# Performance work log

Measured on AMD Instinct MI355X. Metric: run time of the kernel, lower is better.

The kernel has to match this reference:

```python
import jax, jax.numpy as jnp
import numpy as np

B, C, D, H, W = 4, 128, 32, 32, 32
EMB, K = 64, 512


def setup_inputs() -> dict:
    key = jax.random.key(0)
    k1, k2, k3 = jax.random.split(key, 3)
    x = jax.random.normal(k1, (B, C, D, H, W), dtype=jnp.float32)
    conv_w = jax.random.normal(k2, (EMB, C), dtype=jnp.float32) * 0.05  # 1x1x1 Conv3d kernel
    conv_b = jnp.zeros((EMB,), dtype=jnp.float32)
    embed = jax.random.normal(k3, (EMB, K), dtype=jnp.float32)  # codebook, (dim, n_embed)
    return {"x": x, "conv_w": conv_w, "conv_b": conv_b, "embed": embed}


def reference(x, conv_w, conv_b, embed):
    # 1x1x1 Conv3d == per-voxel linear projection; permute to channels-last
    z = jnp.einsum('bcdhw,oc->bdhwo', x, conv_w) + conv_b  # (B,D,H,W,EMB)
    emb_dim = embed.shape[0]
    flat = z.reshape(-1, emb_dim)  # (N, EMB)
    # squared euclidean distance to each codebook entry: ||f||^2 - 2 f.e + ||e||^2
    dist = (jnp.sum(flat * flat, axis=1, keepdims=True)
            - 2.0 * (flat @ embed)
            + jnp.sum(embed * embed, axis=0, keepdims=True))  # (N, K)
    embed_ind = jnp.argmin(dist, axis=1)  # (N,)
    embed_ind = embed_ind.reshape(z.shape[:-1])  # (B,D,H,W)
    quantize = jnp.take(embed.T, embed_ind, axis=0)  # (B,D,H,W,EMB) gather
    diff = jnp.mean((jax.lax.stop_gradient(quantize) - z) ** 2)
    quantize = z + jax.lax.stop_gradient(quantize - z)  # straight-through
    return quantize.transpose(0, 4, 1, 2, 3), diff, embed_ind
```

## Files before the change

### kernel.cpp

```cpp
#include <hip/hip_runtime.h>
#include <hip/hip_bf16.h>

#define CIN   128
#define EMBD  64
#define KC    512
#define SPAT  32768
#define NVOX  131072
#define QSZ   (NVOX * EMBD)
#define DIFF_OFF QSZ
#define IDX_OFF  (QSZ + 1)

__global__ __launch_bounds__(64) void vq_prep(const float* __restrict__ embed,
                                              float* __restrict__ embedT,
                                              float* __restrict__ norms) {
  int k = blockIdx.x;
  int o = threadIdx.x;
  float e = embed[o * KC + k];
  embedT[k * EMBD + o] = e;
  float s = e * e;
  #pragma unroll
  for (int off = 32; off > 0; off >>= 1) s += __shfl_down(s, off);
  if (o == 0) norms[k] = s;
}

__global__ __launch_bounds__(256, 2) void vq_main(
    const float* __restrict__ x, const float* __restrict__ conv_w,
    const float* __restrict__ conv_b, const float* __restrict__ embedT,
    const float* __restrict__ norms, float* __restrict__ out,
    float* __restrict__ partials) {
  __shared__ float wlds[CIN * 68];
  for (int f = threadIdx.x; f < CIN * EMBD; f += 256) {
    int o = f >> 7;
    int c = f & (CIN - 1);
    wlds[c * 68 + o] = conv_w[f];
  }
  __syncthreads();

  const int n = blockIdx.x * 256 + threadIdx.x;
  const int b = n >> 15;
  const int v = n & (SPAT - 1);
  const float* xp = x + ((size_t)b * CIN) * SPAT + v;

  float z[EMBD];
  #pragma unroll
  for (int o = 0; o < EMBD; ++o) z[o] = conv_b[o];

  for (int c = 0; c < CIN; ++c) {
    float xv = xp[(size_t)c * SPAT];
    const float* wr = &wlds[c * 68];
    #pragma unroll
    for (int o = 0; o < EMBD; ++o) z[o] = fmaf(xv, wr[o], z[o]);
  }

  float best = 3.4e38f;
  int bi = 0;
  for (int k = 0; k < KC; ++k) {
    const float* ek = embedT + k * EMBD;
    float d0 = 0.f, d1 = 0.f, d2 = 0.f, d3 = 0.f;
    #pragma unroll
    for (int o = 0; o < EMBD; o += 4) {
      float4 e4 = *(const float4*)(ek + o);
      d0 = fmaf(z[o + 0], e4.x, d0);
      d1 = fmaf(z[o + 1], e4.y, d1);
      d2 = fmaf(z[o + 2], e4.z, d2);
      d3 = fmaf(z[o + 3], e4.w, d3);
    }
    float dot = (d0 + d1) + (d2 + d3);
    float s = fmaf(-2.f, dot, norms[k]);
    if (s < best) { best = s; bi = k; }
  }

  const float* eb = embedT + bi * EMBD;
  float* qout = out + ((size_t)b * EMBD) * SPAT + v;
  float diff = 0.f;
  #pragma unroll
  for (int o = 0; o < EMBD; ++o) {
    float e = eb[o];
    float r = e - z[o];
    diff = fmaf(r, r, diff);
    qout[(size_t)o * SPAT] = e;
  }
  out[IDX_OFF + n] = (float)bi;

  #pragma unroll
  for (int off = 32; off > 0; off >>= 1) diff += __shfl_down(diff, off);
  __syncthreads();
  if ((threadIdx.x & 63) == 0) wlds[threadIdx.x >> 6] = diff;
  __syncthreads();
  if (threadIdx.x == 0)
    partials[blockIdx.x] = wlds[0] + wlds[1] + wlds[2] + wlds[3];
}

__global__ __launch_bounds__(512) void vq_final(const float* __restrict__ partials,
                                                float* __restrict__ out) {
  __shared__ float tmp[8];
  float s = partials[threadIdx.x];
  #pragma unroll
  for (int off = 32; off > 0; off >>= 1) s += __shfl_down(s, off);
  if ((threadIdx.x & 63) == 0) tmp[threadIdx.x >> 6] = s;
  __syncthreads();
  if (threadIdx.x == 0) {
    float t = 0.f;
    #pragma unroll
    for (int i = 0; i < 8; ++i) t += tmp[i];
    out[DIFF_OFF] = t * (1.0f / (float)QSZ);
  }
}

extern "C" void kernel_launch(void* const* d_in, const int* in_sizes, int n_in,
                              void* d_out, int out_size, void* d_ws, size_t ws_size,
                              hipStream_t stream) {
  const float* x      = (const float*)d_in[0];
  const float* conv_w = (const float*)d_in[1];
  const float* conv_b = (const float*)d_in[2];
  const float* embed  = (const float*)d_in[3];
  float* out = (float*)d_out;
  float* ws  = (float*)d_ws;

  float* embedT   = ws;
  float* norms    = ws + 32768;
  float* partials = ws + 33280;

  vq_prep<<<KC, EMBD, 0, stream>>>(embed, embedT, norms);
  vq_main<<<NVOX / 256, 256, 0, stream>>>(x, conv_w, conv_b, embedT, norms,
                                          out, partials);
  vq_final<<<1, 512, 0, stream>>>(partials, out);
}
```

Before: 352.8 us.

## Split embedding dimension across half-waves to cut registers and raise occupancy

Each voxel is now handled by two lanes that each own 32 of the 64 embedding channels, with the partial distance dot product combined through a cross-half shuffle. This halves the per-thread z array, allowing launch bounds of 4 waves per SIMD, and doubles the grid. In exchange each codebook entry needs an extra shuffle per lane, and the x loads are duplicated across the two halves. The LDS weight padding is removed and the final reduction now reads 1024 partials.

```diff
diff --git a/kernel.cpp b/kernel.cpp
--- a/kernel.cpp
+++ b/kernel.cpp
@@ -23,78 +23,88 @@
   if (o == 0) norms[k] = s;
 }
 
-__global__ __launch_bounds__(256, 2) void vq_main(
+__global__ __launch_bounds__(256, 4) void vq_main(
     const float* __restrict__ x, const float* __restrict__ conv_w,
     const float* __restrict__ conv_b, const float* __restrict__ embedT,
     const float* __restrict__ norms, float* __restrict__ out,
     float* __restrict__ partials) {
-  __shared__ float wlds[CIN * 68];
+  __shared__ float wlds[CIN * EMBD];
   for (int f = threadIdx.x; f < CIN * EMBD; f += 256) {
     int o = f >> 7;
     int c = f & (CIN - 1);
-    wlds[c * 68 + o] = conv_w[f];
+    wlds[c * EMBD + o] = conv_w[f];
   }
   __syncthreads();
 
-  const int n = blockIdx.x * 256 + threadIdx.x;
-  const int b = n >> 15;
-  const int v = n & (SPAT - 1);
+  const int tid   = threadIdx.x;
+  const int wv    = tid >> 6;
+  const int lane  = tid & 63;
+  const int h     = lane >> 5;
+  const int vloc  = lane & 31;
+  const int n     = blockIdx.x * 128 + wv * 32 + vloc;
+  const int b     = n >> 15;
+  const int v     = n & (SPAT - 1);
+  const int obase = h * 32;
+
   const float* xp = x + ((size_t)b * CIN) * SPAT + v;
 
-  float z[EMBD];
+  float z[32];
   #pragma unroll
-  for (int o = 0; o < EMBD; ++o) z[o] = conv_b[o];
+  for (int i = 0; i < 32; ++i) z[i] = conv_b[obase + i];
 
+  #pragma unroll 4
   for (int c = 0; c < CIN; ++c) {
     float xv = xp[(size_t)c * SPAT];
-    const float* wr = &wlds[c * 68];
+    const float* wr = &wlds[c * EMBD + obase];
     #pragma unroll
-    for (int o = 0; o < EMBD; ++o) z[o] = fmaf(xv, wr[o], z[o]);
+    for (int i = 0; i < 32; ++i) z[i] = fmaf(xv, wr[i], z[i]);
   }
 
   float best = 3.4e38f;
   int bi = 0;
+  #pragma unroll 2
   for (int k = 0; k < KC; ++k) {
-    const float* ek = embedT + k * EMBD;
+    const float* ek = embedT + k * EMBD + obase;
     float d0 = 0.f, d1 = 0.f, d2 = 0.f, d3 = 0.f;
     #pragma unroll
-    for (int o = 0; o < EMBD; o += 4) {
-      float4 e4 = *(const float4*)(ek + o);
-      d0 = fmaf(z[o + 0], e4.x, d0);
-      d1 = fmaf(z[o + 1], e4.y, d1);
-      d2 = fmaf(z[o + 2], e4.z, d2);
-      d3 = fmaf(z[o + 3], e4.w, d3);
+    for (int q = 0; q < 8; ++q) {
+      float4 e4 = *(const float4*)(ek + q * 4);
+      d0 = fmaf(z[q * 4 + 0], e4.x, d0);
+      d1 = fmaf(z[q * 4 + 1], e4.y, d1);
+      d2 = fmaf(z[q * 4 + 2], e4.z, d2);
+      d3 = fmaf(z[q * 4 + 3], e4.w, d3);
     }
     float dot = (d0 + d1) + (d2 + d3);
+    dot += __shfl_xor(dot, 32);
     float s = fmaf(-2.f, dot, norms[k]);
     if (s < best) { best = s; bi = k; }
   }
 
-  const float* eb = embedT + bi * EMBD;
-  float* qout = out + ((size_t)b * EMBD) * SPAT + v;
+  const float* eb = embedT + bi * EMBD + obase;
+  float* qout = out + ((size_t)b * EMBD + obase) * SPAT + v;
   float diff = 0.f;
   #pragma unroll
-  for (int o = 0; o < EMBD; ++o) {
-    float e = eb[o];
-    float r = e - z[o];
+  for (int i = 0; i < 32; ++i) {
+    float e = eb[i];
+    float r = e - z[i];
     diff = fmaf(r, r, diff);
-    qout[(size_t)o * SPAT] = e;
+    qout[(size_t)i * SPAT] = e;
   }
-  out[IDX_OFF + n] = (float)bi;
+  if (h == 0) out[IDX_OFF + n] = (float)bi;
 
   #pragma unroll
   for (int off = 32; off > 0; off >>= 1) diff += __shfl_down(diff, off);
   __syncthreads();
-  if ((threadIdx.x & 63) == 0) wlds[threadIdx.x >> 6] = diff;
+  if (lane == 0) wlds[wv] = diff;
   __syncthreads();
-  if (threadIdx.x == 0)
+  if (tid == 0)
     partials[blockIdx.x] = wlds[0] + wlds[1] + wlds[2] + wlds[3];
 }
 
 __global__ __launch_bounds__(512) void vq_final(const float* __restrict__ partials,
                                                 float* __restrict__ out) {
   __shared__ float tmp[8];
-  float s = partials[threadIdx.x];
+  float s = partials[threadIdx.x] + partials[threadIdx.x + 512];
   #pragma unroll
   for (int off = 32; off > 0; off >>= 1) s += __shfl_down(s, off);
   if ((threadIdx.x & 63) == 0) tmp[threadIdx.x >> 6] = s;
@@ -122,7 +132,7 @@
   float* partials = ws + 33280;
 
   vq_prep<<<KC, EMBD, 0, stream>>>(embed, embedT, norms);
-  vq_main<<<NVOX / 256, 256, 0, stream>>>(x, conv_w, conv_b, embedT, norms,
+  vq_main<<<NVOX / 128, 256, 0, stream>>>(x, conv_w, conv_b, embedT, norms,
                                           out, partials);
   vq_final<<<1, 512, 0, stream>>>(partials, out);
 }
```

Measured after the change: 640.3 us. +81.5%, slower.

## Compute codebook distances with split-bf16 MFMA and per-block voxel tiling

Applied to the files above, without the earlier changes.

Replaces the scalar per-thread distance loop over all 512 codes with bf16 MFMA matrix products. Both z and the codebook are split into hi/mid/lo bf16 parts, and six cross-product passes approximate fp32 precision. Each block now handles 64 voxels, with the 4 waves each owning 128 codes and 16 output channels. Argmin is reduced via shuffles and LDS, and diff is computed from best distance plus ||z||^2. This removes the heavy VALU dot-product cost, but risks argmin ties or precision mismatches and adds extra prep kernels.

```diff
diff --git a/kernel.cpp b/kernel.cpp
--- a/kernel.cpp
+++ b/kernel.cpp
@@ -9,92 +9,227 @@
 #define QSZ   (NVOX * EMBD)
 #define DIFF_OFF QSZ
 #define IDX_OFF  (QSZ + 1)
-
-__global__ __launch_bounds__(64) void vq_prep(const float* __restrict__ embed,
-                                              float* __restrict__ embedT,
-                                              float* __restrict__ norms) {
+#define NBLK  (NVOX / 64)
+
+typedef __attribute__((ext_vector_type(8))) short bf16x8;
+typedef __attribute__((ext_vector_type(4))) float f32x4;
+
+__device__ __forceinline__ short bf_hi(float f) {
+  __hip_bfloat16 h = __float2bfloat16(f);
+  return *(short*)&h;
+}
+__device__ __forceinline__ float bf_f(short s) {
+  __hip_bfloat16 h = *(__hip_bfloat16*)&s;
+  return __bfloat162float(h);
+}
+
+__global__ __launch_bounds__(64) void vq_prep_e(const float* __restrict__ embed,
+                                                float* __restrict__ embedT,
+                                                float* __restrict__ norms,
+                                                short* __restrict__ e_h,
+                                                short* __restrict__ e_m,
+                                                short* __restrict__ e_l) {
   int k = blockIdx.x;
   int o = threadIdx.x;
   float e = embed[o * KC + k];
   embedT[k * EMBD + o] = e;
+  short h = bf_hi(e);
+  float r1 = e - bf_f(h);
+  short m = bf_hi(r1);
+  short l = bf_hi(r1 - bf_f(m));
+  e_h[k * EMBD + o] = h;
+  e_m[k * EMBD + o] = m;
+  e_l[k * EMBD + o] = l;
   float s = e * e;
   #pragma unroll
   for (int off = 32; off > 0; off >>= 1) s += __shfl_down(s, off);
   if (o == 0) norms[k] = s;
 }
 
+__global__ __launch_bounds__(256) void vq_prep_w(const float* __restrict__ conv_w,
+                                                 float* __restrict__ wT) {
+  int f = blockIdx.x * 256 + threadIdx.x;
+  int c = f >> 6;
+  int o = f & 63;
+  wT[f] = conv_w[o * CIN + c];
+}
+
 __global__ __launch_bounds__(256, 2) void vq_main(
-    const float* __restrict__ x, const float* __restrict__ conv_w,
+    const float* __restrict__ x, const float* __restrict__ wT,
     const float* __restrict__ conv_b, const float* __restrict__ embedT,
-    const float* __restrict__ norms, float* __restrict__ out,
-    float* __restrict__ partials) {
-  __shared__ float wlds[CIN * 68];
-  for (int f = threadIdx.x; f < CIN * EMBD; f += 256) {
-    int o = f >> 7;
-    int c = f & (CIN - 1);
-    wlds[c * 68 + o] = conv_w[f];
-  }
-  __syncthreads();
-
-  const int n = blockIdx.x * 256 + threadIdx.x;
-  const int b = n >> 15;
-  const int v = n & (SPAT - 1);
-  const float* xp = x + ((size_t)b * CIN) * SPAT + v;
-
-  float z[EMBD];
-  #pragma unroll
-  for (int o = 0; o < EMBD; ++o) z[o] = conv_b[o];
-
+    const short* __restrict__ e_h, const short* __restrict__ e_m,
+    const short* __restrict__ e_l, const float* __restrict__ norms,
+    float* __restrict__ out, float* __restrict__ partials) {
+  __shared__ short zh[64 * 64], zm[64 * 64], zl[64 * 64];
+  __shared__ float norml[KC];
+  __shared__ float zsq4[64][4];
+  __shared__ float wbest[4][64];
+  __shared__ int   widx[4][64];
+  __shared__ int   fidx[64];
+
+  const int t    = threadIdx.x;
+  const int q    = t >> 6;
+  const int v    = t & 63;
+  const int n0   = blockIdx.x * 64;
+  const int b    = n0 >> 15;
+  const int vsp  = n0 & (SPAT - 1);
+
+  norml[t]       = norms[t];
+  norml[t + 256] = norms[t + 256];
+
+  const float* xp = x + ((size_t)b * CIN) * SPAT + vsp + v;
+  float z[16];
+  #pragma unroll
+  for (int j = 0; j < 16; ++j) z[j] = conv_b[q * 16 + j];
+
+  #pragma unroll 4
   for (int c = 0; c < CIN; ++c) {
     float xv = xp[(size_t)c * SPAT];
-    const float* wr = &wlds[c * 68];
-    #pragma unroll
-    for (int o = 0; o < EMBD; ++o) z[o] = fmaf(xv, wr[o], z[o]);
-  }
-
-  float best = 3.4e38f;
-  int bi = 0;
-  for (int k = 0; k < KC; ++k) {
-    const float* ek = embedT + k * EMBD;
-    float d0 = 0.f, d1 = 0.f, d2 = 0.f, d3 = 0.f;
-    #pragma unroll
-    for (int o = 0; o < EMBD; o += 4) {
-      float4 e4 = *(const float4*)(ek + o);
-      d0 = fmaf(z[o + 0], e4.x, d0);
-      d1 = fmaf(z[o + 1], e4.y, d1);
-      d2 = fmaf(z[o + 2], e4.z, d2);
-      d3 = fmaf(z[o + 3], e4.w, d3);
-    }
-    float dot = (d0 + d1) + (d2 + d3);
-    float s = fmaf(-2.f, dot, norms[k]);
-    if (s < best) { best = s; bi = k; }
-  }
-
-  const float* eb = embedT + bi * EMBD;
-  float* qout = out + ((size_t)b * EMBD) * SPAT + v;
-  float diff = 0.f;
-  #pragma unroll
-  for (int o = 0; o < EMBD; ++o) {
-    float e = eb[o];
-    float r = e - z[o];
-    diff = fmaf(r, r, diff);
-    qout[(size_t)o * SPAT] = e;
-  }
-  out[IDX_OFF + n] = (float)bi;
-
-  #pragma unroll
-  for (int off = 32; off > 0; off >>= 1) diff += __shfl_down(diff, off);
-  __syncthreads();
-  if ((threadIdx.x & 63) == 0) wlds[threadIdx.x >> 6] = diff;
-  __syncthreads();
-  if (threadIdx.x == 0)
-    partials[blockIdx.x] = wlds[0] + wlds[1] + wlds[2] + wlds[3];
+    const float* wr = wT + c * EMBD + q * 16;
+    #pragma unroll
+    for (int j = 0; j < 16; ++j) z[j] = fmaf(xv, wr[j], z[j]);
+  }
+
+  float sq = 0.f;
+  #pragma unroll
+  for (int j = 0; j < 16; ++j) sq = fmaf(z[j], z[j], sq);
+  zsq4[v][q] = sq;
+
+  short h16[16], m16[16], l16[16];
+  #pragma unroll
+  for (int j = 0; j < 16; ++j) {
+    short h = bf_hi(z[j]);
+    float r1 = z[j] - bf_f(h);
+    short m = bf_hi(r1);
+    h16[j] = h; m16[j] = m; l16[j] = bf_hi(r1 - bf_f(m));
+  }
+  #pragma unroll
+  for (int jj = 0; jj < 2; ++jj) {
+    int s = (2 * q + jj) ^ (v & 7);
+    int byte = v * 128 + s * 16;
+    bf16x8 hv, mv, lv;
+    #pragma unroll
+    for (int j = 0; j < 8; ++j) { hv[j] = h16[jj*8+j]; mv[j] = m16[jj*8+j]; lv[j] = l16[jj*8+j]; }
+    *(bf16x8*)((char*)zh + byte) = hv;
+    *(bf16x8*)((char*)zm + byte) = mv;
+    *(bf16x8*)((char*)zl + byte) = lv;
+  }
+  __syncthreads();
+
+  const int lane = t & 63;
+  const int l15  = lane & 15;
+  const int g    = lane >> 4;
+
+  f32x4 acc[4][8];
+  #pragma unroll
+  for (int m = 0; m < 4; ++m)
+    #pragma unroll
+    for (int n = 0; n < 8; ++n) { f32x4 z4 = {0.f,0.f,0.f,0.f}; acc[m][n] = z4; }
+
+  const int boff = (q * 128 + l15) * 128 + g * 16;
+
+  auto dist_pass = [&](const short* zlds, const short* __restrict__ eg) {
+    #pragma unroll
+    for (int ks8 = 0; ks8 <= 4; ks8 += 4) {
+      bf16x8 a[4];
+      #pragma unroll
+      for (int m = 0; m < 4; ++m) {
+        int vox = m * 16 + l15;
+        a[m] = *(const bf16x8*)((const char*)zlds + vox * 128 +
+                                (((ks8 + g) ^ (vox & 7)) << 4));
+      }
+      #pragma unroll
+      for (int n = 0; n < 8; ++n) {
+        bf16x8 bb = *(const bf16x8*)((const char*)eg + boff + n * 2048 + ks8 * 16);
+        #pragma unroll
+        for (int m = 0; m < 4; ++m)
+          acc[m][n] = __builtin_amdgcn_mfma_f32_16x16x32_bf16(a[m], bb, acc[m][n], 0, 0, 0);
+      }
+    }
+  };
+  dist_pass(zh, e_h);
+  dist_pass(zh, e_m);
+  dist_pass(zm, e_h);
+  dist_pass(zh, e_l);
+  dist_pass(zl, e_h);
+  dist_pass(zm, e_m);
+
+  float nv[8];
+  #pragma unroll
+  for (int n = 0; n < 8; ++n) nv[n] = norml[q * 128 + n * 16 + l15];
+
+  float best[16]; int bidx[16];
+  #pragma unroll
+  for (int i = 0; i < 16; ++i) { best[i] = 3.4e38f; bidx[i] = 0; }
+  #pragma unroll
+  for (int n = 0; n < 8; ++n)
+    #pragma unroll
+    for (int m = 0; m < 4; ++m)
+      #pragma unroll
+      for (int r = 0; r < 4; ++r) {
+        float s = fmaf(-2.f, acc[m][n][r], nv[n]);
+        int code = q * 128 + n * 16 + l15;
+        int i = m * 4 + r;
+        bool tk = s < best[i];
+        best[i] = tk ? s : best[i];
+        bidx[i] = tk ? code : bidx[i];
+      }
+  #pragma unroll
+  for (int i = 0; i < 16; ++i) {
+    #pragma unroll
+    for (int d = 1; d < 16; d <<= 1) {
+      float os = __shfl_xor(best[i], d);
+      int   oi = __shfl_xor(bidx[i], d);
+      bool tk = (os < best[i]) || (os == best[i] && oi < bidx[i]);
+      best[i] = tk ? os : best[i];
+      bidx[i] = tk ? oi : bidx[i];
+    }
+  }
+  if (l15 == 0) {
+    #pragma unroll
+    for (int i = 0; i < 16; ++i) {
+      int vox = (i >> 2) * 16 + g * 4 + (i & 3);
+      wbest[q][vox] = best[i];
+      widx[q][vox]  = bidx[i];
+    }
+  }
+  __syncthreads();
+
+  if (t < 64) {
+    float bs = wbest[0][t]; int bi = widx[0][t];
+    #pragma unroll
+    for (int w2 = 1; w2 < 4; ++w2) {
+      float s2 = wbest[w2][t]; int i2 = widx[w2][t];
+      bool tk = (s2 < bs) || (s2 == bs && i2 < bi);
+      bs = tk ? s2 : bs; bi = tk ? i2 : bi;
+    }
+    fidx[t] = bi;
+    out[IDX_OFF + n0 + t] = (float)bi;
+    float d = bs + zsq4[t][0] + zsq4[t][1] + zsq4[t][2] + zsq4[t][3];
+    #pragma unroll
+    for (int off = 32; off > 0; off >>= 1) d += __shfl_down(d, off);
+    if (t == 0) partials[blockIdx.x] = d;
+  }
+  __syncthreads();
+
+  const int bi = fidx[v];
+  const float* er = embedT + bi * EMBD + q * 16;
+  float* qout = out + ((size_t)b * EMBD + q * 16) * SPAT + vsp + v;
+  #pragma unroll
+  for (int u = 0; u < 4; ++u) {
+    float4 e4 = *(const float4*)(er + u * 4);
+    qout[(size_t)(u * 4 + 0) * SPAT] = e4.x;
+    qout[(size_t)(u * 4 + 1) * SPAT] = e4.y;
+    qout[(size_t)(u * 4 + 2) * SPAT] = e4.z;
+    qout[(size_t)(u * 4 + 3) * SPAT] = e4.w;
+  }
 }
 
 __global__ __launch_bounds__(512) void vq_final(const float* __restrict__ partials,
                                                 float* __restrict__ out) {
   __shared__ float tmp[8];
-  float s = partials[threadIdx.x];
+  float s = partials[threadIdx.x] + partials[threadIdx.x + 512] +
+            partials[threadIdx.x + 1024] + partials[threadIdx.x + 1536];
   #pragma unroll
   for (int off = 32; off > 0; off >>= 1) s += __shfl_down(s, off);
   if ((threadIdx.x & 63) == 0) tmp[threadIdx.x >> 6] = s;
@@ -119,10 +254,15 @@
 
   float* embedT   = ws;
   float* norms    = ws + 32768;
-  float* partials = ws + 33280;
-
-  vq_prep<<<KC, EMBD, 0, stream>>>(embed, embedT, norms);
-  vq_main<<<NVOX / 256, 256, 0, stream>>>(x, conv_w, conv_b, embedT, norms,
-                                          out, partials);
+  float* wT       = ws + 33280;
+  float* partials = ws + 41472;
+  short* e_h      = (short*)(ws + 43520);
+  short* e_m      = e_h + KC * EMBD;
+  short* e_l      = e_m + KC * EMBD;
+
+  vq_prep_e<<<KC, EMBD, 0, stream>>>(embed, embedT, norms, e_h, e_m, e_l);
+  vq_prep_w<<<32, 256, 0, stream>>>(conv_w, wT);
+  vq_main<<<NBLK, 256, 0, stream>>>(x, wT, conv_b, embedT, e_h, e_m, e_l,
+                                    norms, out, partials);
   vq_final<<<1, 512, 0, stream>>>(partials, out);
 }
```

New measurement: 403.5 us. 14.4% more time.
